# Kernel optimization log

Hardware: AMD Instinct MI355X
Metric: run time of the kernel (lower is better)

The kernel has to match this reference:

```python
import jax, jax.numpy as jnp
import numpy as np

# ---- Cl(3,0) algebra tables (basis: 1, e1, e2, e3, e12, e13, e23, e123) ----
def _build_algebra():
    dim = 8
    blades = sorted(range(dim), key=lambda b: (bin(b).count('1'), b))
    idx = {b: i for i, b in enumerate(blades)}
    C = np.zeros((dim, dim, dim), np.float32)
    for a in range(dim):
        for b in range(dim):
            s = 0; ash = a >> 1
            while ash:
                s += bin(ash & b).count('1'); ash >>= 1
            C[idx[a], idx[b], idx[a ^ b]] = -1.0 if (s & 1) else 1.0
    grades = np.array([bin(b).count('1') for b in blades])
    rev = np.array([(-1.0) ** (g * (g - 1) // 2) for g in grades], np.float32)
    gmask = np.zeros((4, dim), np.float32)
    gmask[grades, np.arange(dim)] = 1.0
    return C, rev, gmask, grades

_C_np, _REV_np, _GM_np, _GRADES = _build_algebra()
CAYLEY = jnp.asarray(_C_np)          # [8,8,8] sparse multiplication table
REV = jnp.asarray(_REV_np)           # reverse signs per blade
GMASK = jnp.asarray(_GM_np)          # [4,8] grade selector
BV_IDX = jnp.asarray(np.where(_GRADES == 2)[0])  # bivector slots [4,5,6]
G1_IDX = jnp.asarray(np.where(_GRADES == 1)[0])  # vector slots [1,2,3]

EPS = 1e-6
H_NUM, DEPTH, A_NUM, DISC, TEMP = 8, 3, 5, 0.99, 1.0

def gp(a, b):
    return jnp.einsum('...i,...j,ijk->...k', a, b, CAYLEY)

def reverse(x):
    return x * REV

def grade_energy(x):  # [...,8] -> [...,4] per-grade sum of squares
    return jnp.einsum('...d,gd->...g', x * x, GMASK)

def scatter_bv(c):  # [...,3] bivector coeffs -> full multivector [...,8]
    out = jnp.zeros(c.shape[:-1] + (8,), c.dtype)
    return out.at[..., BV_IDX].set(c)

def mv_exp_biv(b):  # exp of pure bivector in Cl(3,0): cos|B| + sinc|B| * B
    t = jnp.sqrt(jnp.sum(b * b, -1))
    small = t < 1e-6
    ts = jnp.where(small, 1.0, t)
    sinc = jnp.where(small, 1.0 - t * t / 6.0, jnp.sin(ts) / ts)
    return (sinc[..., None] * b).at[..., 0].add(jnp.cos(t))

def clayernorm(x, w):  # normalize by mean multivector norm across channels
    n = jnp.sqrt(jnp.sum(x * x, -1) + EPS)          # [...,C]
    denom = jnp.mean(n, -1, keepdims=True)[..., None] + EPS
    return x * w[:, None] / denom

def ggelu(x):  # gate multivector by GELU of its norm
    n = jnp.sqrt(jnp.sum(x * x, -1, keepdims=True) + EPS)
    return x * jax.nn.gelu(n) / (n + EPS)

def clinear(x, W, b):  # channel-mixing per blade: [O,C]x[...,C,8]
    return jnp.einsum('oc,...cd->...od', W, x) + b

def rotor_apply(x, bv):  # per-channel rotor sandwich, bv [C,3]
    R = mv_exp_biv(-0.5 * scatter_bv(bv))  # [C,8]
    return gp(gp(R, x), reverse(R))

def predict(x, nw, lw, lb, vw, vb, pw, pb):
    h = clayernorm(x, nw)
    h = clinear(h, lw, lb)
    h = ggelu(h)
    value = h[..., 0] @ vw + vb                      # grade-0 -> [N,1]
    g1 = h[..., G1_IDX].reshape(h.shape[0], -1)       # grade-1 flat
    policy = g1 @ pw + pb                             # [N,A]
    return policy, value

def dynamics(x, action, act_bv, nw, rbv, lw, lb, rw, rb):
    bv = act_bv[action]                               # [N,3]
    R = mv_exp_biv(-0.5 * scatter_bv(bv))[:, None, :]  # [N,1,8]
    ns = gp(gp(R, x), reverse(R))                     # rotor sandwich
    h = clayernorm(ns, nw)
    h = ggelu(h)
    h = rotor_apply(h, rbv)
    h = clinear(h, lw, lb)
    ns = ns + h                                       # residual GA block
    reward = ns[..., 0] @ rw + rb
    return reward, ns


def setup_inputs() -> dict:
    key = jax.random.key(0)
    ks = jax.random.split(key, 16)
    B, C, mid = 512, 256, 128
    f = jnp.float32
    return {
        'state': jax.random.normal(ks[0], (B, C, 8), f),
        'hyp_bv': jax.random.normal(ks[1], (H_NUM, 3), f) * 0.05,
        'sp_w1': jax.random.normal(ks[2], (4, 32), f) * 0.3,
        'sp_b1': jnp.zeros((32,), f),
        'sp_w2': jax.random.normal(ks[3], (32, 1), f) * 0.3,
        'sp_b2': jnp.zeros((1,), f),
        'p_norm_w': jnp.ones((C,), f),
        'p_lin_w': jax.random.normal(ks[4], (mid, C), f) / np.sqrt(C),
        'p_lin_b': jnp.zeros((mid, 8), f),
        'p_vw': jax.random.normal(ks[5], (mid, 1), f) * 0.1,
        'p_vb': jnp.zeros((1,), f),
        'p_pw': jax.random.normal(ks[6], (mid * 3, A_NUM), f) * 0.1,
        'p_pb': jnp.zeros((A_NUM,), f),
        'act_bv': jax.random.normal(ks[7], (A_NUM, 3), f) * 0.1,
        'd_norm_w': jnp.ones((C,), f),
        'd_rotor_bv': jax.random.normal(ks[8], (C, 3), f) * 0.05,
        'd_lin_w': jax.random.normal(ks[9], (C, C), f) / np.sqrt(C),
        'd_lin_b': jnp.zeros((C, 8), f),
        'd_rw': jax.random.normal(ks[10], (C, 1), f) * 0.1,
        'd_rb': jnp.zeros((1,), f),
    }


def reference(state, hyp_bv, sp_w1, sp_b1, sp_w2, sp_b2,
              p_norm_w, p_lin_w, p_lin_b, p_vw, p_vb, p_pw, p_pb,
              act_bv, d_norm_w, d_rotor_bv, d_lin_w, d_lin_b, d_rw, d_rb):
    B, C, D = state.shape
    H, A = H_NUM, A_NUM
    # hypothesis generation: H independent rotors applied to state
    R = mv_exp_biv(-0.5 * scatter_bv(hyp_bv))          # [H,8]
    hyp = gp(gp(R[None, :, None, :], state[:, None, :, :]),
             reverse(R)[None, :, None, :])             # [B,H,C,8]
    # exploration parameter from grade-norm features
    norms = jnp.sqrt(grade_energy(state) + 1e-12)       # [B,C,4]
    pooled = norms.mean(1)                              # [B,4]
    theta = jnp.maximum(pooled @ sp_w1 + sp_b1, 0.0) @ sp_w2 + sp_b2
    explore = jnp.abs(jnp.tanh(theta))                  # [B,1]
    N = B * H
    hf = hyp.reshape(N, C, D)
    exp_bh = jnp.broadcast_to(explore[:, None, :], (B, H, 1)).reshape(N, 1)
    noise = jax.random.normal(jax.random.key(42), (DEPTH, N, A), state.dtype) * 0.3
    hyp_values = jnp.zeros((B, H), state.dtype)
    first_actions = jnp.zeros((N,), jnp.int32)
    for d in range(DEPTH):  # fixed small depth loop; H vectorized
        policy, value = predict(hf, p_norm_w, p_lin_w, p_lin_b, p_vw, p_vb, p_pw, p_pb)
        bv_e = grade_energy(hf)[:, :, 2].mean(1, keepdims=True)  # bivector energy
        scores = policy + exp_bh * bv_e * noise[d]
        action = jnp.argmax(scores, -1)
        if d == 0:
            first_actions = action
        reward, hf = dynamics(hf, action, act_bv, d_norm_w, d_rotor_bv,
                              d_lin_w, d_lin_b, d_rw, d_rb)
        hyp_values = hyp_values + (DISC ** d) * reward.reshape(B, H)
    _, tv = predict(hf, p_norm_w, p_lin_w, p_lin_b, p_vw, p_vb, p_pw, p_pb)
    hyp_values = hyp_values + (DISC ** DEPTH) * tv.reshape(B, H)
    weights = jax.nn.softmax(hyp_values / TEMP, -1)     # [B,H]
    oh = jax.nn.one_hot(first_actions.reshape(B, H), A, dtype=state.dtype)
    ap = jnp.sum(weights[..., None] * oh, 1)            # [B,A]
    return ap / jnp.clip(jnp.sum(ap, -1, keepdims=True), 1e-8)
```

## Files before the change

### kernel.cpp

```cpp
#include <hip/hip_runtime.h>
#include <math.h>


#define NOISE_MODE 0
#define DEV static __device__ __forceinline__

constexpr int Bz = 512;
constexpr int Cz = 256;
constexpr int MIDz = 128;
constexpr int Hz = 8;
constexpr int Nz = 4096;
constexpr int Az = 5;
constexpr int NOISE_PER_D = Nz * Az;

constexpr size_t OFF_ROTH  = 0;
constexpr size_t OFF_ROTA  = OFF_ROTH + 64;
constexpr size_t OFF_ROTC  = OFF_ROTA + 40;
constexpr size_t OFF_EXPL  = OFF_ROTC + 2048;
constexpr size_t OFF_HV    = OFF_EXPL + 512;
constexpr size_t OFF_ACT   = OFF_HV + 4096;
constexpr size_t OFF_FIRST = OFF_ACT + 4096;
constexpr size_t OFF_WTP   = OFF_FIRST + 4096;
constexpr size_t OFF_WTD   = OFF_WTP + (size_t)Cz * MIDz;
constexpr size_t OFF_A     = OFF_WTD + (size_t)Cz * Cz;
constexpr size_t OFF_B     = OFF_A + (size_t)Nz * Cz * 8;

DEV void gp8(const float* a, const float* b, float* c) {
  c[0] = a[0]*b[0]+a[1]*b[1]+a[2]*b[2]+a[3]*b[3]-a[4]*b[4]-a[5]*b[5]-a[6]*b[6]-a[7]*b[7];
  c[1] = a[0]*b[1]+a[1]*b[0]-a[2]*b[4]-a[3]*b[5]+a[4]*b[2]+a[5]*b[3]-a[6]*b[7]-a[7]*b[6];
  c[2] = a[0]*b[2]+a[2]*b[0]+a[1]*b[4]-a[4]*b[1]-a[3]*b[6]+a[6]*b[3]+a[5]*b[7]+a[7]*b[5];
  c[3] = a[0]*b[3]+a[3]*b[0]+a[1]*b[5]-a[5]*b[1]+a[2]*b[6]-a[6]*b[2]-a[4]*b[7]-a[7]*b[4];
  c[4] = a[0]*b[4]+a[4]*b[0]+a[1]*b[2]-a[2]*b[1]-a[5]*b[6]+a[6]*b[5]+a[3]*b[7]+a[7]*b[3];
  c[5] = a[0]*b[5]+a[5]*b[0]+a[1]*b[3]-a[3]*b[1]+a[4]*b[6]-a[6]*b[4]-a[2]*b[7]-a[7]*b[2];
  c[6] = a[0]*b[6]+a[6]*b[0]+a[2]*b[3]-a[3]*b[2]-a[4]*b[5]+a[5]*b[4]+a[1]*b[7]+a[7]*b[1];
  c[7] = a[0]*b[7]+a[7]*b[0]+a[1]*b[6]+a[6]*b[1]+a[3]*b[4]+a[4]*b[3]-a[2]*b[5]-a[5]*b[2];
}

DEV void sandwich8(const float* R, const float* x, float* y) {
  float t[8];
  gp8(R, x, t);
  float Rr[8] = {R[0], R[1], R[2], R[3], -R[4], -R[5], -R[6], -R[7]};
  gp8(t, Rr, y);
}

DEV void rotor_from_bv(const float* bv, float* R) {
  float c4 = -0.5f * bv[0], c5 = -0.5f * bv[1], c6 = -0.5f * bv[2];
  float t = sqrtf(c4*c4 + c5*c5 + c6*c6);
  float sinc = (t < 1e-6f) ? (1.0f - t*t/6.0f) : (sinf(t)/t);
  R[0] = cosf(t); R[1] = 0.f; R[2] = 0.f; R[3] = 0.f;
  R[4] = sinc*c4; R[5] = sinc*c5; R[6] = sinc*c6; R[7] = 0.f;
}

DEV unsigned tf_rotl(unsigned v, int n) { return (v << n) | (v >> (32 - n)); }

DEV void threefry2x32(unsigned x0, unsigned x1, unsigned& o0, unsigned& o1) {
  const unsigned k0 = 0u, k1 = 42u;
  const unsigned k2 = k0 ^ k1 ^ 0x1BD11BDAu;
  x0 += k0; x1 += k1;
#define TF_R(r) { x0 += x1; x1 = tf_rotl(x1, r); x1 ^= x0; }
  TF_R(13) TF_R(15) TF_R(26) TF_R(6)
  x0 += k1; x1 += k2 + 1u;
  TF_R(17) TF_R(29) TF_R(16) TF_R(24)
  x0 += k2; x1 += k0 + 2u;
  TF_R(13) TF_R(15) TF_R(26) TF_R(6)
  x0 += k0; x1 += k1 + 3u;
  TF_R(17) TF_R(29) TF_R(16) TF_R(24)
  x0 += k1; x1 += k2 + 4u;
  TF_R(13) TF_R(15) TF_R(26) TF_R(6)
  x0 += k2; x1 += k0 + 5u;
#undef TF_R
  o0 = x0; o1 = x1;
}

DEV float erfinv32(float x) {
  float w = -log1pf(-x * x);
  float p;
  if (w < 5.0f) {
    w = w - 2.5f;
    p = 2.81022636e-08f;
    p = fmaf(p, w, 3.43273939e-07f);
    p = fmaf(p, w, -3.5233877e-06f);
    p = fmaf(p, w, -4.39150654e-06f);
    p = fmaf(p, w, 0.00021858087f);
    p = fmaf(p, w, -0.00125372503f);
    p = fmaf(p, w, -0.00417768164f);
    p = fmaf(p, w, 0.246640727f);
    p = fmaf(p, w, 1.50140941f);
  } else {
    w = sqrtf(w) - 3.0f;
    p = -0.000200214257f;
    p = fmaf(p, w, 0.000100950558f);
    p = fmaf(p, w, 0.00134934322f);
    p = fmaf(p, w, -0.00367342844f);
    p = fmaf(p, w, 0.00573950773f);
    p = fmaf(p, w, -0.0076224613f);
    p = fmaf(p, w, 0.00943887047f);
    p = fmaf(p, w, 1.00167406f);
    p = fmaf(p, w, 2.83297682f);
  }
  return p * x;
}

DEV float noise_val(int d, int r, int a) {
  unsigned idx = (unsigned)(d * NOISE_PER_D + r * Az + a);
  unsigned o0, o1, bits;
#if NOISE_MODE == 0
  threefry2x32(0u, idx, o0, o1);
  bits = o0 ^ o1;
#elif NOISE_MODE == 1
  const unsigned HALF = (unsigned)(3 * NOISE_PER_D) / 2u;
  unsigned j = (idx < HALF) ? idx : idx - HALF;
  threefry2x32(j, j + HALF, o0, o1);
  bits = (idx < HALF) ? o0 : o1;
#elif NOISE_MODE == 2
  threefry2x32(0u, idx, o0, o1);
  bits = o1;
#else
  threefry2x32(0u, idx, o0, o1);
  bits = o0;
#endif
  const float MINV = __uint_as_float(0xBF7FFFFFu);
  float f = __uint_as_float((bits >> 9) | 0x3F800000u) - 1.0f;
  float u = fmaxf(MINV, f * 2.0f + MINV);
  const float SQRT2 = __uint_as_float(0x3FB504F3u);
  return (SQRT2 * erfinv32(u)) * 0.3f;
}

DEV float gelu_tanh(float x) {
  float x3 = (x * x) * x;
  float t = tanhf(0.7978845608028654f * (x + 0.044715f * x3));
  return x * (0.5f * (1.0f + t));
}


__global__ void k_prep(const float* __restrict__ hyp_bv, const float* __restrict__ act_bv,
                       const float* __restrict__ rot_bv, const float* __restrict__ plw,
                       const float* __restrict__ pnw, const float* __restrict__ dlw,
                       float* __restrict__ rotH, float* __restrict__ rotA,
                       float* __restrict__ rotC, float* __restrict__ hyp_val,
                       float* __restrict__ WtP, float* __restrict__ WtD) {
  int t = blockIdx.x * 256 + threadIdx.x;
  if (t < Cz * Cz)   { int c = t >> 8, o = t & 255; WtD[t] = dlw[o * Cz + c]; }
  if (t < Cz * MIDz) { int c = t >> 7, o = t & 127; WtP[t] = plw[o * Cz + c] * pnw[c]; }
  if (t < Nz) hyp_val[t] = 0.f;
  if (t < 8) rotor_from_bv(hyp_bv + t * 3, rotH + t * 8);
  else if (t < 13) rotor_from_bv(act_bv + (t - 8) * 3, rotA + (t - 8) * 8);
  else if (t >= 16 && t < 16 + Cz) rotor_from_bv(rot_bv + (t - 16) * 3, rotC + (t - 16) * 8);
}

__global__ void k_explore(const float* __restrict__ state, const float* __restrict__ w1,
                          const float* __restrict__ b1, const float* __restrict__ w2,
                          const float* __restrict__ b2, float* __restrict__ explore) {
  int b = blockIdx.x, c = threadIdx.x;
  const float4* xp = (const float4*)(state + ((size_t)b * Cz + c) * 8);
  float4 lo = xp[0], hi = xp[1];
  float g0 = lo.x * lo.x;
  float g1 = lo.y * lo.y + lo.z * lo.z + lo.w * lo.w;
  float g2 = hi.x * hi.x + hi.y * hi.y + hi.z * hi.z;
  float g3 = hi.w * hi.w;
  __shared__ float4 sm[256];
  sm[c] = make_float4(sqrtf(g0 + 1e-12f), sqrtf(g1 + 1e-12f),
                      sqrtf(g2 + 1e-12f), sqrtf(g3 + 1e-12f));
  __syncthreads();
  for (int s = 128; s > 0; s >>= 1) {
    if (c < s) {
      sm[c].x += sm[c + s].x; sm[c].y += sm[c + s].y;
      sm[c].z += sm[c + s].z; sm[c].w += sm[c + s].w;
    }
    __syncthreads();
  }
  if (c == 0) {
    float pooled[4] = {sm[0].x / 256.f, sm[0].y / 256.f, sm[0].z / 256.f, sm[0].w / 256.f};
    float theta = b2[0];
    for (int j = 0; j < 32; j++) {
      float hj = b1[j];
      for (int g = 0; g < 4; g++) hj = fmaf(pooled[g], w1[g * 32 + j], hj);
      hj = fmaxf(hj, 0.f);
      theta = fmaf(hj, w2[j], theta);
    }
    explore[b] = fabsf(tanhf(theta));
  }
}

__global__ __launch_bounds__(256) void k_pred(
    const float* __restrict__ src, int apply_hyp, int dstep, int mode,
    const float* __restrict__ rotH, const float* __restrict__ WtP,
    const float* __restrict__ lb, const float* __restrict__ pw,
    const float* __restrict__ pb, const float* __restrict__ vw,
    const float* __restrict__ vb, const float* __restrict__ explore,
    float* __restrict__ hyp_val, int* __restrict__ action,
    int* __restrict__ first_act, float termdisc) {
  __shared__ float4 xs[4][2 * Cz];
  int w = threadIdx.x >> 6, l = threadIdx.x & 63;
  int r = blockIdx.x * 4 + w;
  int b = r >> 3, h = r & 7;
  const float* row = apply_hyp ? (src + (size_t)b * Cz * 8) : (src + (size_t)r * Cz * 8);
  float Rh[8];
  if (apply_hyp) {
#pragma unroll
    for (int i = 0; i < 8; i++) Rh[i] = rotH[h * 8 + i];
  }
  float nsum = 0.f, bsum = 0.f;
#pragma unroll
  for (int g = 0; g < 4; g++) {
    int c = l + 64 * g;
    const float4* xp = (const float4*)(row + (size_t)c * 8);
    float4 v0 = xp[0], v1 = xp[1];
    float x[8] = {v0.x, v0.y, v0.z, v0.w, v1.x, v1.y, v1.z, v1.w};
    if (apply_hyp) {
      float y[8];
      sandwich8(Rh, x, y);
#pragma unroll
      for (int i = 0; i < 8; i++) x[i] = y[i];
    }
    float ss = 0.f;
#pragma unroll
    for (int i = 0; i < 8; i++) ss += x[i] * x[i];
    nsum += sqrtf(ss + 1e-6f);
    bsum += x[4] * x[4] + x[5] * x[5] + x[6] * x[6];
    xs[w][c]      = make_float4(x[0], x[1], x[2], x[3]);
    xs[w][Cz + c] = make_float4(x[4], x[5], x[6], x[7]);
  }
#pragma unroll
  for (int m = 1; m < 64; m <<= 1) {
    nsum += __shfl_xor(nsum, m);
    bsum += __shfl_xor(bsum, m);
  }
  float invd = 1.0f / (nsum / 256.f + 1e-6f);
  float bv_e = bsum / 256.f;

  float acc[2][8] = {{0,0,0,0,0,0,0,0},{0,0,0,0,0,0,0,0}};
#pragma unroll 2
  for (int c = 0; c < Cz; c++) {
    float4 xa = xs[w][c], xb = xs[w][Cz + c];
    float xv[8] = {xa.x, xa.y, xa.z, xa.w, xb.x, xb.y, xb.z, xb.w};
    float w0 = WtP[(size_t)c * MIDz + l];
    float w1v = WtP[(size_t)c * MIDz + l + 64];
#pragma unroll
    for (int dd = 0; dd < 8; dd++) {
      acc[0][dd] = fmaf(w0, xv[dd], acc[0][dd]);
      acc[1][dd] = fmaf(w1v, xv[dd], acc[1][dd]);
    }
  }
  float hh[2][8];
#pragma unroll
  for (int j = 0; j < 2; j++) {
    int o = l + 64 * j;
    float nsq = 0.f;
#pragma unroll
    for (int dd = 0; dd < 8; dd++) {
      hh[j][dd] = acc[j][dd] * invd + lb[o * 8 + dd];
      nsq += hh[j][dd] * hh[j][dd];
    }
    float nn = sqrtf(nsq + 1e-6f);
    float sc = gelu_tanh(nn) / (nn + 1e-6f);
#pragma unroll
    for (int dd = 0; dd < 8; dd++) hh[j][dd] *= sc;
  }
  if (mode == 0) {
    float pol[Az] = {0, 0, 0, 0, 0};
#pragma unroll
    for (int j = 0; j < 2; j++) {
      int o = l + 64 * j;
#pragma unroll
      for (int k = 0; k < 3; k++) {
        float v = hh[j][1 + k];
        const float* pwj = pw + (size_t)(o * 3 + k) * Az;
#pragma unroll
        for (int a = 0; a < Az; a++) pol[a] = fmaf(v, pwj[a], pol[a]);
      }
    }
#pragma unroll
    for (int m = 1; m < 64; m <<= 1) {
#pragma unroll
      for (int a = 0; a < Az; a++) pol[a] += __shfl_xor(pol[a], m);
    }
    if (l == 0) {
      float coef = explore[b] * bv_e;
      int best = 0;
      float bs = -INFINITY;
      for (int a = 0; a < Az; a++) {
        float s = pol[a] + pb[a] + coef * noise_val(dstep, r, a);
        if (s > bs) { bs = s; best = a; }
      }
      action[r] = best;
      if (dstep == 0) first_act[r] = best;
    }
  } else {
    float v = 0.f;
#pragma unroll
    for (int j = 0; j < 2; j++) v = fmaf(hh[j][0], vw[l + 64 * j], v);
#pragma unroll
    for (int m = 1; m < 64; m <<= 1) v += __shfl_xor(v, m);
    if (l == 0) hyp_val[r] += termdisc * (v + vb[0]);
  }
}

__global__ __launch_bounds__(256) void k_dyn(
    const float* __restrict__ src, float* __restrict__ dst, int apply_hyp,
    const int* __restrict__ action, const float* __restrict__ rotH,
    const float* __restrict__ rotA, const float* __restrict__ rotC,
    const float* __restrict__ dnw, const float* __restrict__ WtD,
    const float* __restrict__ lb, const float* __restrict__ rw,
    const float* __restrict__ rb, float* __restrict__ hyp_val, float discf) {
  __shared__ float4 xs[4][2 * Cz];
  int w = threadIdx.x >> 6, l = threadIdx.x & 63;
  int r = blockIdx.x * 4 + w;
  int b = r >> 3, h = r & 7;
  const float* row = apply_hyp ? (src + (size_t)b * Cz * 8) : (src + (size_t)r * Cz * 8);
  int a = action[r];
  float Ra[8];
#pragma unroll
  for (int i = 0; i < 8; i++) Ra[i] = rotA[a * 8 + i];
  float Rh[8];
  if (apply_hyp) {
#pragma unroll
    for (int i = 0; i < 8; i++) Rh[i] = rotH[h * 8 + i];
  }
  float y[4][8];
  float nsum = 0.f;
#pragma unroll
  for (int g = 0; g < 4; g++) {
    int c = l + 64 * g;
    const float4* xp = (const float4*)(row + (size_t)c * 8);
    float4 v0 = xp[0], v1 = xp[1];
    float x[8] = {v0.x, v0.y, v0.z, v0.w, v1.x, v1.y, v1.z, v1.w};
    if (apply_hyp) {
      float t[8];
      sandwich8(Rh, x, t);
#pragma unroll
      for (int i = 0; i < 8; i++) x[i] = t[i];
    }
    sandwich8(Ra, x, y[g]);
    float ss = 0.f;
#pragma unroll
    for (int i = 0; i < 8; i++) ss += y[g][i] * y[g][i];
    nsum += sqrtf(ss + 1e-6f);
  }
#pragma unroll
  for (int m = 1; m < 64; m <<= 1) nsum += __shfl_xor(nsum, m);
  float invd = 1.0f / (nsum / 256.f + 1e-6f);
#pragma unroll
  for (int g = 0; g < 4; g++) {
    int c = l + 64 * g;
    float sc = dnw[c] * invd;
    float hch[8];
    float nsq = 0.f;
#pragma unroll
    for (int i = 0; i < 8; i++) { hch[i] = y[g][i] * sc; nsq += hch[i] * hch[i]; }
    float nn = sqrtf(nsq + 1e-6f);
    float ge = gelu_tanh(nn) / (nn + 1e-6f);
#pragma unroll
    for (int i = 0; i < 8; i++) hch[i] *= ge;
    float Rc[8];
    const float4* rp = (const float4*)(rotC + (size_t)c * 8);
    float4 r0 = rp[0], r1 = rp[1];
    Rc[0] = r0.x; Rc[1] = r0.y; Rc[2] = r0.z; Rc[3] = r0.w;
    Rc[4] = r1.x; Rc[5] = r1.y; Rc[6] = r1.z; Rc[7] = r1.w;
    float hp[8];
    sandwich8(Rc, hch, hp);
    xs[w][c]      = make_float4(hp[0], hp[1], hp[2], hp[3]);
    xs[w][Cz + c] = make_float4(hp[4], hp[5], hp[6], hp[7]);
  }
  float acc[4][8] = {{0,0,0,0,0,0,0,0},{0,0,0,0,0,0,0,0},
                     {0,0,0,0,0,0,0,0},{0,0,0,0,0,0,0,0}};
#pragma unroll 2
  for (int c = 0; c < Cz; c++) {
    float4 xa = xs[w][c], xb = xs[w][Cz + c];
    float xv[8] = {xa.x, xa.y, xa.z, xa.w, xb.x, xb.y, xb.z, xb.w};
#pragma unroll
    for (int g = 0; g < 4; g++) {
      float wv = WtD[(size_t)c * Cz + l + 64 * g];
#pragma unroll
      for (int dd = 0; dd < 8; dd++) acc[g][dd] = fmaf(wv, xv[dd], acc[g][dd]);
    }
  }
  float rsum = 0.f;
  float* drow = dst + (size_t)r * Cz * 8;
#pragma unroll
  for (int g = 0; g < 4; g++) {
    int o = l + 64 * g;
    float out[8];
#pragma unroll
    for (int dd = 0; dd < 8; dd++)
      out[dd] = y[g][dd] + (acc[g][dd] + lb[o * 8 + dd]);
    float4* op = (float4*)(drow + (size_t)o * 8);
    op[0] = make_float4(out[0], out[1], out[2], out[3]);
    op[1] = make_float4(out[4], out[5], out[6], out[7]);
    rsum = fmaf(out[0], rw[o], rsum);
  }
#pragma unroll
  for (int m = 1; m < 64; m <<= 1) rsum += __shfl_xor(rsum, m);
  if (l == 0) hyp_val[r] += discf * (rsum + rb[0]);
}

__global__ void k_out(const float* __restrict__ hyp_val, const int* __restrict__ first_act,
                      float* __restrict__ out) {
  int b = blockIdx.x * blockDim.x + threadIdx.x;
  if (b >= Bz) return;
  float hv[Hz];
  float m = -INFINITY;
#pragma unroll
  for (int h = 0; h < Hz; h++) { hv[h] = hyp_val[b * Hz + h]; m = fmaxf(m, hv[h]); }
  float e[Hz];
  float se = 0.f;
#pragma unroll
  for (int h = 0; h < Hz; h++) { e[h] = expf(hv[h] - m); se += e[h]; }
  float ap[Az] = {0, 0, 0, 0, 0};
#pragma unroll
  for (int h = 0; h < Hz; h++) ap[first_act[b * Hz + h]] += e[h] / se;
  float tot = 0.f;
#pragma unroll
  for (int a = 0; a < Az; a++) tot += ap[a];
  float dn = fmaxf(tot, 1e-8f);
#pragma unroll
  for (int a = 0; a < Az; a++) out[b * Az + a] = ap[a] / dn;
}


extern "C" void kernel_launch(void* const* d_in, const int* in_sizes, int n_in,
                              void* d_out, int out_size, void* d_ws, size_t ws_size,
                              hipStream_t stream) {
  const float* state      = (const float*)d_in[0];
  const float* hyp_bv     = (const float*)d_in[1];
  const float* sp_w1      = (const float*)d_in[2];
  const float* sp_b1      = (const float*)d_in[3];
  const float* sp_w2      = (const float*)d_in[4];
  const float* sp_b2      = (const float*)d_in[5];
  const float* p_norm_w   = (const float*)d_in[6];
  const float* p_lin_w    = (const float*)d_in[7];
  const float* p_lin_b    = (const float*)d_in[8];
  const float* p_vw       = (const float*)d_in[9];
  const float* p_vb       = (const float*)d_in[10];
  const float* p_pw       = (const float*)d_in[11];
  const float* p_pb       = (const float*)d_in[12];
  const float* act_bv     = (const float*)d_in[13];
  const float* d_norm_w   = (const float*)d_in[14];
  const float* d_rotor_bv = (const float*)d_in[15];
  const float* d_lin_w    = (const float*)d_in[16];
  const float* d_lin_b    = (const float*)d_in[17];
  const float* d_rw       = (const float*)d_in[18];
  const float* d_rb       = (const float*)d_in[19];
  float* out = (float*)d_out;
  float* ws  = (float*)d_ws;

  float* rotH    = ws + OFF_ROTH;
  float* rotA    = ws + OFF_ROTA;
  float* rotC    = ws + OFF_ROTC;
  float* explore = ws + OFF_EXPL;
  float* hyp_val = ws + OFF_HV;
  int*   action  = (int*)(ws + OFF_ACT);
  int*   first   = (int*)(ws + OFF_FIRST);
  float* WtP     = ws + OFF_WTP;
  float* WtD     = ws + OFF_WTD;
  float* bufA    = ws + OFF_A;
  float* bufB    = ws + OFF_B;

  k_prep<<<256, 256, 0, stream>>>(hyp_bv, act_bv, d_rotor_bv, p_lin_w, p_norm_w,
                                  d_lin_w, rotH, rotA, rotC, hyp_val, WtP, WtD);
  k_explore<<<Bz, 256, 0, stream>>>(state, sp_w1, sp_b1, sp_w2, sp_b2, explore);

  const float discp[4] = {1.0f, 0.99f, (float)(0.99 * 0.99), (float)(0.99 * 0.99 * 0.99)};
  const float* cur = state;
  float* nxt = bufA;
  for (int d = 0; d < 3; d++) {
    int ah = (d == 0) ? 1 : 0;
    k_pred<<<Nz / 4, 256, 0, stream>>>(cur, ah, d, 0, rotH, WtP, p_lin_b, p_pw, p_pb,
                                       p_vw, p_vb, explore, hyp_val, action, first, 0.f);
    k_dyn<<<Nz / 4, 256, 0, stream>>>(cur, nxt, ah, action, rotH, rotA, rotC, d_norm_w,
                                      WtD, d_lin_b, d_rw, d_rb, hyp_val, discp[d]);
    cur = nxt;
    nxt = (d == 0) ? bufB : ((d == 1) ? bufA : bufB);
  }
  k_pred<<<Nz / 4, 256, 0, stream>>>(cur, 0, 0, 1, rotH, WtP, p_lin_b, p_pw, p_pb,
                                     p_vw, p_vb, explore, hyp_val, action, first,
                                     discp[3]);
  k_out<<<2, 256, 0, stream>>>(hyp_val, first, out);
}
```

Before: 464.6 us.

## Fuse predict and dynamics into one per-row step kernel with terminal value

Merges the separate predict and dynamics kernels into a single k_step kernel with one 64-thread block per hypothesis row. The rotated row is kept in LDS, so policy, argmax, action rotor, layer norm and the dynamics GEMM all run without re-reading the row from global memory or passing actions through a buffer. The last step also computes the terminal value prediction in place and never writes its state out. The in-place bufA update is safe because each block reads only its own row, and this removes the second buffer. In exchange, blocks are smaller (launch bounds 64,4), which may lower occupancy and weight reuse across waves in a block.

New measurement: 904.0 us. +94.6%, slower.

```diff
diff --git a/kernel.cpp b/kernel.cpp
--- a/kernel.cpp
+++ b/kernel.cpp
@@ -18,12 +18,10 @@
 constexpr size_t OFF_ROTC  = OFF_ROTA + 40;
 constexpr size_t OFF_EXPL  = OFF_ROTC + 2048;
 constexpr size_t OFF_HV    = OFF_EXPL + 512;
-constexpr size_t OFF_ACT   = OFF_HV + 4096;
-constexpr size_t OFF_FIRST = OFF_ACT + 4096;
+constexpr size_t OFF_FIRST = OFF_HV + 4096;
 constexpr size_t OFF_WTP   = OFF_FIRST + 4096;
 constexpr size_t OFF_WTD   = OFF_WTP + (size_t)Cz * MIDz;
 constexpr size_t OFF_A     = OFF_WTD + (size_t)Cz * Cz;
-constexpr size_t OFF_B     = OFF_A + (size_t)Nz * Cz * 8;
 
 DEV void gp8(const float* a, const float* b, float* c) {
   c[0] = a[0]*b[0]+a[1]*b[1]+a[2]*b[2]+a[3]*b[3]-a[4]*b[4]-a[5]*b[5]-a[6]*b[6]-a[7]*b[7];
@@ -132,6 +130,38 @@
   return x * (0.5f * (1.0f + t));
 }
 
+DEV void pred_gemm(const float4* __restrict__ xs, int l, float invd,
+                   const float* __restrict__ WtP, const float* __restrict__ plb,
+                   float hh[2][8]) {
+  float pacc[2][8] = {{0,0,0,0,0,0,0,0},{0,0,0,0,0,0,0,0}};
+#pragma unroll 4
+  for (int c = 0; c < Cz; c++) {
+    float4 xa = xs[c], xb = xs[Cz + c];
+    float xv[8] = {xa.x, xa.y, xa.z, xa.w, xb.x, xb.y, xb.z, xb.w};
+    float w0 = WtP[(size_t)c * MIDz + l];
+    float w1 = WtP[(size_t)c * MIDz + 64 + l];
+#pragma unroll
+    for (int dd = 0; dd < 8; dd++) {
+      pacc[0][dd] = fmaf(w0, xv[dd], pacc[0][dd]);
+      pacc[1][dd] = fmaf(w1, xv[dd], pacc[1][dd]);
+    }
+  }
+#pragma unroll
+  for (int j = 0; j < 2; j++) {
+    int o = l + 64 * j;
+    float nsq = 0.f;
+#pragma unroll
+    for (int dd = 0; dd < 8; dd++) {
+      hh[j][dd] = fmaf(pacc[j][dd], invd, plb[o * 8 + dd]);
+      nsq += hh[j][dd] * hh[j][dd];
+    }
+    float nn = sqrtf(nsq + 1e-6f);
+    float sc = gelu_tanh(nn) / (nn + 1e-6f);
+#pragma unroll
+    for (int dd = 0; dd < 8; dd++) hh[j][dd] *= sc;
+  }
+}
+
 
 __global__ void k_prep(const float* __restrict__ hyp_bv, const float* __restrict__ act_bv,
                        const float* __restrict__ rot_bv, const float* __restrict__ plw,
@@ -182,17 +212,21 @@
   }
 }
 
-__global__ __launch_bounds__(256) void k_pred(
-    const float* __restrict__ src, int apply_hyp, int dstep, int mode,
-    const float* __restrict__ rotH, const float* __restrict__ WtP,
-    const float* __restrict__ lb, const float* __restrict__ pw,
+__global__ __launch_bounds__(64, 4) void k_step(
+    const float* __restrict__ src, float* __restrict__ dst, int apply_hyp,
+    int dstep, int do_term,
+    const float* __restrict__ rotH, const float* __restrict__ rotA,
+    const float* __restrict__ rotC, const float* __restrict__ WtP,
+    const float* __restrict__ plb, const float* __restrict__ pw,
     const float* __restrict__ pb, const float* __restrict__ vw,
-    const float* __restrict__ vb, const float* __restrict__ explore,
-    float* __restrict__ hyp_val, int* __restrict__ action,
-    int* __restrict__ first_act, float termdisc) {
-  __shared__ float4 xs[4][2 * Cz];
-  int w = threadIdx.x >> 6, l = threadIdx.x & 63;
-  int r = blockIdx.x * 4 + w;
+    const float* __restrict__ vb, const float* __restrict__ dnw,
+    const float* __restrict__ WtD, const float* __restrict__ dlb,
+    const float* __restrict__ rw, const float* __restrict__ rb,
+    const float* __restrict__ explore, float* __restrict__ hyp_val,
+    int* __restrict__ first_act, float discf, float termdisc) {
+  __shared__ float4 xs[2 * Cz];
+  int l = threadIdx.x;
+  int r = blockIdx.x;
   int b = r >> 3, h = r & 7;
   const float* row = apply_hyp ? (src + (size_t)b * Cz * 8) : (src + (size_t)r * Cz * 8);
   float Rh[8];
@@ -201,124 +235,6 @@
     for (int i = 0; i < 8; i++) Rh[i] = rotH[h * 8 + i];
   }
   float nsum = 0.f, bsum = 0.f;
-#pragma unroll
-  for (int g = 0; g < 4; g++) {
-    int c = l + 64 * g;
-    const float4* xp = (const float4*)(row + (size_t)c * 8);
-    float4 v0 = xp[0], v1 = xp[1];
-    float x[8] = {v0.x, v0.y, v0.z, v0.w, v1.x, v1.y, v1.z, v1.w};
-    if (apply_hyp) {
-      float y[8];
-      sandwich8(Rh, x, y);
-#pragma unroll
-      for (int i = 0; i < 8; i++) x[i] = y[i];
-    }
-    float ss = 0.f;
-#pragma unroll
-    for (int i = 0; i < 8; i++) ss += x[i] * x[i];
-    nsum += sqrtf(ss + 1e-6f);
-    bsum += x[4] * x[4] + x[5] * x[5] + x[6] * x[6];
-    xs[w][c]      = make_float4(x[0], x[1], x[2], x[3]);
-    xs[w][Cz + c] = make_float4(x[4], x[5], x[6], x[7]);
-  }
-#pragma unroll
-  for (int m = 1; m < 64; m <<= 1) {
-    nsum += __shfl_xor(nsum, m);
-    bsum += __shfl_xor(bsum, m);
-  }
-  float invd = 1.0f / (nsum / 256.f + 1e-6f);
-  float bv_e = bsum / 256.f;
-
-  float acc[2][8] = {{0,0,0,0,0,0,0,0},{0,0,0,0,0,0,0,0}};
-#pragma unroll 2
-  for (int c = 0; c < Cz; c++) {
-    float4 xa = xs[w][c], xb = xs[w][Cz + c];
-    float xv[8] = {xa.x, xa.y, xa.z, xa.w, xb.x, xb.y, xb.z, xb.w};
-    float w0 = WtP[(size_t)c * MIDz + l];
-    float w1v = WtP[(size_t)c * MIDz + l + 64];
-#pragma unroll
-    for (int dd = 0; dd < 8; dd++) {
-      acc[0][dd] = fmaf(w0, xv[dd], acc[0][dd]);
-      acc[1][dd] = fmaf(w1v, xv[dd], acc[1][dd]);
-    }
-  }
-  float hh[2][8];
-#pragma unroll
-  for (int j = 0; j < 2; j++) {
-    int o = l + 64 * j;
-    float nsq = 0.f;
-#pragma unroll
-    for (int dd = 0; dd < 8; dd++) {
-      hh[j][dd] = acc[j][dd] * invd + lb[o * 8 + dd];
-      nsq += hh[j][dd] * hh[j][dd];
-    }
-    float nn = sqrtf(nsq + 1e-6f);
-    float sc = gelu_tanh(nn) / (nn + 1e-6f);
-#pragma unroll
-    for (int dd = 0; dd < 8; dd++) hh[j][dd] *= sc;
-  }
-  if (mode == 0) {
-    float pol[Az] = {0, 0, 0, 0, 0};
-#pragma unroll
-    for (int j = 0; j < 2; j++) {
-      int o = l + 64 * j;
-#pragma unroll
-      for (int k = 0; k < 3; k++) {
-        float v = hh[j][1 + k];
-        const float* pwj = pw + (size_t)(o * 3 + k) * Az;
-#pragma unroll
-        for (int a = 0; a < Az; a++) pol[a] = fmaf(v, pwj[a], pol[a]);
-      }
-    }
-#pragma unroll
-    for (int m = 1; m < 64; m <<= 1) {
-#pragma unroll
-      for (int a = 0; a < Az; a++) pol[a] += __shfl_xor(pol[a], m);
-    }
-    if (l == 0) {
-      float coef = explore[b] * bv_e;
-      int best = 0;
-      float bs = -INFINITY;
-      for (int a = 0; a < Az; a++) {
-        float s = pol[a] + pb[a] + coef * noise_val(dstep, r, a);
-        if (s > bs) { bs = s; best = a; }
-      }
-      action[r] = best;
-      if (dstep == 0) first_act[r] = best;
-    }
-  } else {
-    float v = 0.f;
-#pragma unroll
-    for (int j = 0; j < 2; j++) v = fmaf(hh[j][0], vw[l + 64 * j], v);
-#pragma unroll
-    for (int m = 1; m < 64; m <<= 1) v += __shfl_xor(v, m);
-    if (l == 0) hyp_val[r] += termdisc * (v + vb[0]);
-  }
-}
-
-__global__ __launch_bounds__(256) void k_dyn(
-    const float* __restrict__ src, float* __restrict__ dst, int apply_hyp,
-    const int* __restrict__ action, const float* __restrict__ rotH,
-    const float* __restrict__ rotA, const float* __restrict__ rotC,
-    const float* __restrict__ dnw, const float* __restrict__ WtD,
-    const float* __restrict__ lb, const float* __restrict__ rw,
-    const float* __restrict__ rb, float* __restrict__ hyp_val, float discf) {
-  __shared__ float4 xs[4][2 * Cz];
-  int w = threadIdx.x >> 6, l = threadIdx.x & 63;
-  int r = blockIdx.x * 4 + w;
-  int b = r >> 3, h = r & 7;
-  const float* row = apply_hyp ? (src + (size_t)b * Cz * 8) : (src + (size_t)r * Cz * 8);
-  int a = action[r];
-  float Ra[8];
-#pragma unroll
-  for (int i = 0; i < 8; i++) Ra[i] = rotA[a * 8 + i];
-  float Rh[8];
-  if (apply_hyp) {
-#pragma unroll
-    for (int i = 0; i < 8; i++) Rh[i] = rotH[h * 8 + i];
-  }
-  float y[4][8];
-  float nsum = 0.f;
 #pragma unroll
   for (int g = 0; g < 4; g++) {
     int c = l + 64 * g;
@@ -331,19 +247,79 @@
 #pragma unroll
       for (int i = 0; i < 8; i++) x[i] = t[i];
     }
+    float ss = 0.f;
+#pragma unroll
+    for (int i = 0; i < 8; i++) ss += x[i] * x[i];
+    nsum += sqrtf(ss + 1e-6f);
+    bsum += x[4] * x[4] + x[5] * x[5] + x[6] * x[6];
+    xs[c]      = make_float4(x[0], x[1], x[2], x[3]);
+    xs[Cz + c] = make_float4(x[4], x[5], x[6], x[7]);
+  }
+#pragma unroll
+  for (int m = 1; m < 64; m <<= 1) {
+    nsum += __shfl_xor(nsum, m);
+    bsum += __shfl_xor(bsum, m);
+  }
+  float invd = 1.0f / (nsum / 256.f + 1e-6f);
+  float bv_e = bsum / 256.f;
+  __syncthreads();
+
+  float hh[2][8];
+  pred_gemm(xs, l, invd, WtP, plb, hh);
+  float pol[Az] = {0, 0, 0, 0, 0};
+#pragma unroll
+  for (int j = 0; j < 2; j++) {
+    int o = l + 64 * j;
+#pragma unroll
+    for (int k = 0; k < 3; k++) {
+      float v = hh[j][1 + k];
+      const float* pwj = pw + (size_t)(o * 3 + k) * Az;
+#pragma unroll
+      for (int a = 0; a < Az; a++) pol[a] = fmaf(v, pwj[a], pol[a]);
+    }
+  }
+#pragma unroll
+  for (int m = 1; m < 64; m <<= 1) {
+#pragma unroll
+    for (int a = 0; a < Az; a++) pol[a] += __shfl_xor(pol[a], m);
+  }
+  int best = 0;
+  if (l == 0) {
+    float coef = explore[b] * bv_e;
+    float bs = -INFINITY;
+    for (int a = 0; a < Az; a++) {
+      float s = pol[a] + pb[a] + coef * noise_val(dstep, r, a);
+      if (s > bs) { bs = s; best = a; }
+    }
+    if (dstep == 0) first_act[r] = best;
+  }
+  best = __shfl(best, 0);
+
+  float Ra[8];
+#pragma unroll
+  for (int i = 0; i < 8; i++) Ra[i] = rotA[best * 8 + i];
+  float y[4][8];
+  float nsum2 = 0.f;
+#pragma unroll
+  for (int g = 0; g < 4; g++) {
+    int c = l + 64 * g;
+    float4 xa = xs[c], xb = xs[Cz + c];
+    float x[8] = {xa.x, xa.y, xa.z, xa.w, xb.x, xb.y, xb.z, xb.w};
     sandwich8(Ra, x, y[g]);
     float ss = 0.f;
 #pragma unroll
     for (int i = 0; i < 8; i++) ss += y[g][i] * y[g][i];
-    nsum += sqrtf(ss + 1e-6f);
-  }
-#pragma unroll
-  for (int m = 1; m < 64; m <<= 1) nsum += __shfl_xor(nsum, m);
-  float invd = 1.0f / (nsum / 256.f + 1e-6f);
+    nsum2 += sqrtf(ss + 1e-6f);
+  }
+#pragma unroll
+  for (int m = 1; m < 64; m <<= 1) nsum2 += __shfl_xor(nsum2, m);
+  float invd2 = 1.0f / (nsum2 / 256.f + 1e-6f);
+  __syncthreads();
+
 #pragma unroll
   for (int g = 0; g < 4; g++) {
     int c = l + 64 * g;
-    float sc = dnw[c] * invd;
+    float sc = dnw[c] * invd2;
     float hch[8];
     float nsq = 0.f;
 #pragma unroll
@@ -359,39 +335,66 @@
     Rc[4] = r1.x; Rc[5] = r1.y; Rc[6] = r1.z; Rc[7] = r1.w;
     float hp[8];
     sandwich8(Rc, hch, hp);
-    xs[w][c]      = make_float4(hp[0], hp[1], hp[2], hp[3]);
-    xs[w][Cz + c] = make_float4(hp[4], hp[5], hp[6], hp[7]);
-  }
+    xs[c]      = make_float4(hp[0], hp[1], hp[2], hp[3]);
+    xs[Cz + c] = make_float4(hp[4], hp[5], hp[6], hp[7]);
+  }
+  __syncthreads();
+
   float acc[4][8] = {{0,0,0,0,0,0,0,0},{0,0,0,0,0,0,0,0},
                      {0,0,0,0,0,0,0,0},{0,0,0,0,0,0,0,0}};
-#pragma unroll 2
+#pragma unroll 4
   for (int c = 0; c < Cz; c++) {
-    float4 xa = xs[w][c], xb = xs[w][Cz + c];
+    float4 xa = xs[c], xb = xs[Cz + c];
     float xv[8] = {xa.x, xa.y, xa.z, xa.w, xb.x, xb.y, xb.z, xb.w};
 #pragma unroll
     for (int g = 0; g < 4; g++) {
-      float wv = WtD[(size_t)c * Cz + l + 64 * g];
+      float wv = WtD[(size_t)c * Cz + 64 * g + l];
 #pragma unroll
       for (int dd = 0; dd < 8; dd++) acc[g][dd] = fmaf(wv, xv[dd], acc[g][dd]);
     }
   }
-  float rsum = 0.f;
+
+  if (do_term) __syncthreads();
+  float rsum = 0.f, tsum = 0.f;
   float* drow = dst + (size_t)r * Cz * 8;
 #pragma unroll
   for (int g = 0; g < 4; g++) {
     int o = l + 64 * g;
     float out[8];
-#pragma unroll
-    for (int dd = 0; dd < 8; dd++)
-      out[dd] = y[g][dd] + (acc[g][dd] + lb[o * 8 + dd]);
-    float4* op = (float4*)(drow + (size_t)o * 8);
-    op[0] = make_float4(out[0], out[1], out[2], out[3]);
-    op[1] = make_float4(out[4], out[5], out[6], out[7]);
+    float ss = 0.f;
+#pragma unroll
+    for (int dd = 0; dd < 8; dd++) {
+      out[dd] = y[g][dd] + (acc[g][dd] + dlb[o * 8 + dd]);
+      ss += out[dd] * out[dd];
+    }
     rsum = fmaf(out[0], rw[o], rsum);
+    if (do_term) {
+      tsum += sqrtf(ss + 1e-6f);
+      xs[o]      = make_float4(out[0], out[1], out[2], out[3]);
+      xs[Cz + o] = make_float4(out[4], out[5], out[6], out[7]);
+    } else {
+      float4* op = (float4*)(drow + (size_t)o * 8);
+      op[0] = make_float4(out[0], out[1], out[2], out[3]);
+      op[1] = make_float4(out[4], out[5], out[6], out[7]);
+    }
   }
 #pragma unroll
   for (int m = 1; m < 64; m <<= 1) rsum += __shfl_xor(rsum, m);
-  if (l == 0) hyp_val[r] += discf * (rsum + rb[0]);
+  float hv_add = discf * (rsum + rb[0]);
+
+  if (do_term) {
+#pragma unroll
+    for (int m = 1; m < 64; m <<= 1) tsum += __shfl_xor(tsum, m);
+    float invd3 = 1.0f / (tsum / 256.f + 1e-6f);
+    __syncthreads();
+    float th[2][8];
+    pred_gemm(xs, l, invd3, WtP, plb, th);
+    float v = fmaf(th[0][0], vw[l], th[1][0] * vw[l + 64]);
+#pragma unroll
+    for (int m = 1; m < 64; m <<= 1) v += __shfl_xor(v, m);
+    hv_add += termdisc * (v + vb[0]);
+  }
+  if (l == 0) hyp_val[r] += hv_add;
 }
 
 __global__ void k_out(const float* __restrict__ hyp_val, const int* __restrict__ first_act,
@@ -449,31 +452,24 @@
   float* rotC    = ws + OFF_ROTC;
   float* explore = ws + OFF_EXPL;
   float* hyp_val = ws + OFF_HV;
-  int*   action  = (int*)(ws + OFF_ACT);
   int*   first   = (int*)(ws + OFF_FIRST);
   float* WtP     = ws + OFF_WTP;
   float* WtD     = ws + OFF_WTD;
   float* bufA    = ws + OFF_A;
-  float* bufB    = ws + OFF_B;
 
   k_prep<<<256, 256, 0, stream>>>(hyp_bv, act_bv, d_rotor_bv, p_lin_w, p_norm_w,
                                   d_lin_w, rotH, rotA, rotC, hyp_val, WtP, WtD);
   k_explore<<<Bz, 256, 0, stream>>>(state, sp_w1, sp_b1, sp_w2, sp_b2, explore);
 
-  const float discp[4] = {1.0f, 0.99f, (float)(0.99 * 0.99), (float)(0.99 * 0.99 * 0.99)};
-  const float* cur = state;
-  float* nxt = bufA;
-  for (int d = 0; d < 3; d++) {
-    int ah = (d == 0) ? 1 : 0;
-    k_pred<<<Nz / 4, 256, 0, stream>>>(cur, ah, d, 0, rotH, WtP, p_lin_b, p_pw, p_pb,
-                                       p_vw, p_vb, explore, hyp_val, action, first, 0.f);
-    k_dyn<<<Nz / 4, 256, 0, stream>>>(cur, nxt, ah, action, rotH, rotA, rotC, d_norm_w,
-                                      WtD, d_lin_b, d_rw, d_rb, hyp_val, discp[d]);
-    cur = nxt;
-    nxt = (d == 0) ? bufB : ((d == 1) ? bufA : bufB);
-  }
-  k_pred<<<Nz / 4, 256, 0, stream>>>(cur, 0, 0, 1, rotH, WtP, p_lin_b, p_pw, p_pb,
-                                     p_vw, p_vb, explore, hyp_val, action, first,
-                                     discp[3]);
+  const float d1 = 0.99f, d2 = 0.99f * 0.99f, d3 = 0.99f * 0.99f * 0.99f;
+  k_step<<<Nz, 64, 0, stream>>>(state, bufA, 1, 0, 0, rotH, rotA, rotC, WtP, p_lin_b,
+                                p_pw, p_pb, p_vw, p_vb, d_norm_w, WtD, d_lin_b,
+                                d_rw, d_rb, explore, hyp_val, first, 1.0f, 0.f);
+  k_step<<<Nz, 64, 0, stream>>>(bufA, bufA, 0, 1, 0, rotH, rotA, rotC, WtP, p_lin_b,
+                                p_pw, p_pb, p_vw, p_vb, d_norm_w, WtD, d_lin_b,
+                                d_rw, d_rb, explore, hyp_val, first, d1, 0.f);
+  k_step<<<Nz, 64, 0, stream>>>(bufA, bufA, 0, 2, 1, rotH, rotA, rotC, WtP, p_lin_b,
+                                p_pw, p_pb, p_vw, p_vb, d_norm_w, WtD, d_lin_b,
+                                d_rw, d_rb, explore, hyp_val, first, d2, d3);
   k_out<<<2, 256, 0, stream>>>(hyp_val, first, out);
 }
```
